# Optimization experiments

Hardware: AMD Instinct MI355X
Metric: run time of the kernel (lower is better)

## Reference

```python
import jax, jax.numpy as jnp
import numpy as np

B = 65536
D = 764  # n_dim


def setup_inputs() -> dict:
    key = jax.random.key(0)
    k1, k2, k3 = jax.random.split(key, 3)
    x = jax.random.normal(k1, (B, D), dtype=jnp.float32)
    # Packed weights: row i holds linear_layers[i].weight (length max(1,i), zero-padded).
    W = jax.random.normal(k2, (D, D), dtype=jnp.float32) * 0.02
    b = jax.random.normal(k3, (D,), dtype=jnp.float32) * 0.02
    return {"x": x, "W": W, "b": b}


def reference(x, W, b):
    # Original: output[i] = x[:, :i] @ W_i^T + b_i for i>=1; output[0] = b_0
    # (layer 0 is applied to an explicit zeros tensor, so its weight contributes nothing).
    # This is a single strictly-lower-triangular masked matmul.
    d = W.shape[0]
    mask = jnp.tril(jnp.ones((d, d), dtype=x.dtype), k=-1)  # row i uses cols < i
    return jnp.einsum('bd,nd->bn', x, W * mask) + b  # [B, n_dim]
```

## Files before the change

### kernel.cpp

```cpp
#include <hip/hip_runtime.h>

#define D_DIM 764
#define DP    768
#define BM    128
#define BN    128
#define BK    64

typedef __attribute__((ext_vector_type(8))) short bf16x8;
typedef __attribute__((ext_vector_type(8))) unsigned short u16x8;
typedef __attribute__((ext_vector_type(4))) float f32x4;

typedef __attribute__((address_space(3))) char lds_char;
typedef __attribute__((address_space(1))) const char g_char;

__device__ inline unsigned short f2bf(float f) {
    union { float f; unsigned u; } v; v.f = f;
    unsigned r = v.u + 0x7FFFu + ((v.u >> 16) & 1u);
    return (unsigned short)(r >> 16);
}

__global__ void prep_w(const float* __restrict__ W, unsigned short* __restrict__ Wb) {
    int idx = blockIdx.x * blockDim.x + threadIdx.x;
    int n = idx / DP, k = idx - n * DP;
    float v = 0.0f;
    if (n < D_DIM && k < n) v = W[n * D_DIM + k];
    Wb[idx] = f2bf(v);
}

__global__ __launch_bounds__(256, 4) void fvsbn_gemm(
    const float* __restrict__ X,
    const unsigned short* __restrict__ Wb,
    const float* __restrict__ bias,
    float* __restrict__ out)
{
    __shared__ __align__(16) unsigned short As[BM * BK];
    __shared__ __align__(16) unsigned short Bs[BN * BK];

    const int tid  = threadIdx.x;
    const int lane = tid & 63;
    const int wid  = tid >> 6;
    const int wm   = wid & 1;
    const int wn   = wid >> 1;
    const int quad = lane >> 4;
    const int l16  = lane & 15;

    const int bid = blockIdx.x;
    const int xcd = bid & 7;
    const int j   = bid >> 3;
    const int nt  = j % 6;
    const int jm  = j / 6;
    const int mt  = jm * 8 + xcd;
    const int m0  = mt * BM;
    const int n0  = nt * BN;

    const int num_k = (n0 + BN) / BK;

    f32x4 acc[4][4];
#pragma unroll
    for (int i = 0; i < 4; ++i)
#pragma unroll
        for (int jj = 0; jj < 4; ++jj) acc[i][jj] = (f32x4){0.f, 0.f, 0.f, 0.f};

    for (int kk = 0; kk < num_k; ++kk) {
        const int k0 = kk * BK;

#pragma unroll
        for (int jj = 0; jj < 4; ++jj) {
            const int cbase = (wid * 4 + jj) * 64;
            const int c     = cbase + lane;
            const int r     = c >> 3;
            const int cc    = c & 7;
            const int g     = cc ^ (r & 7);
            const unsigned short* gp = Wb + (size_t)(n0 + r) * DP + k0 + g * 8;
            __builtin_amdgcn_global_load_lds((g_char*)gp,
                                             (lds_char*)((char*)Bs + cbase * 16),
                                             16, 0, 0);
        }

#pragma unroll
        for (int i = 0; i < 4; ++i) {
            const int p  = tid + i * 256;
            const int r  = p >> 3;
            const int cc = p & 7;
            const int g  = cc ^ (r & 7);
            const int k  = k0 + g * 8;
            const float* xp = X + (size_t)(m0 + r) * D_DIM + k;
            float4 lo = *(const float4*)xp;
            float4 hi = (k + 8 <= D_DIM) ? *(const float4*)(xp + 4)
                                         : make_float4(0.f, 0.f, 0.f, 0.f);
            u16x8 pk;
            pk[0] = f2bf(lo.x); pk[1] = f2bf(lo.y); pk[2] = f2bf(lo.z); pk[3] = f2bf(lo.w);
            pk[4] = f2bf(hi.x); pk[5] = f2bf(hi.y); pk[6] = f2bf(hi.z); pk[7] = f2bf(hi.w);
            *(u16x8*)&As[r * BK + cc * 8] = pk;
        }

        __syncthreads();

#pragma unroll
        for (int s = 0; s < 2; ++s) {
            bf16x8 af[4], bfr[4];
#pragma unroll
            for (int mi = 0; mi < 4; ++mi) {
                const int r = wm * 64 + mi * 16 + l16;
                const int g = s * 4 + quad;
                af[mi] = *(const bf16x8*)&As[r * BK + (g ^ (r & 7)) * 8];
            }
#pragma unroll
            for (int ni = 0; ni < 4; ++ni) {
                const int r = wn * 64 + ni * 16 + l16;
                const int g = s * 4 + quad;
                bfr[ni] = *(const bf16x8*)&Bs[r * BK + (g ^ (r & 7)) * 8];
            }
#pragma unroll
            for (int mi = 0; mi < 4; ++mi)
#pragma unroll
                for (int ni = 0; ni < 4; ++ni)
                    acc[mi][ni] = __builtin_amdgcn_mfma_f32_16x16x32_bf16(
                        af[mi], bfr[ni], acc[mi][ni], 0, 0, 0);
        }

        __syncthreads();
    }

#pragma unroll
    for (int ni = 0; ni < 4; ++ni) {
        const int col = n0 + wn * 64 + ni * 16 + l16;
        if (col < D_DIM) {
            const float bv = bias[col];
#pragma unroll
            for (int mi = 0; mi < 4; ++mi) {
                const int row = m0 + wm * 64 + mi * 16 + quad * 4;
#pragma unroll
                for (int r = 0; r < 4; ++r)
                    out[(size_t)(row + r) * D_DIM + col] = acc[mi][ni][r] + bv;
            }
        }
    }
}

extern "C" void kernel_launch(void* const* d_in, const int* in_sizes, int n_in,
                              void* d_out, int out_size, void* d_ws, size_t ws_size,
                              hipStream_t stream) {
    const float* X    = (const float*)d_in[0];
    const float* W    = (const float*)d_in[1];
    const float* bias = (const float*)d_in[2];
    float* out        = (float*)d_out;
    unsigned short* Wb = (unsigned short*)d_ws;

    prep_w<<<(DP * DP) / 256, 256, 0, stream>>>(W, Wb);
    fvsbn_gemm<<<(65536 / BM) * (DP / BN), 256, 0, stream>>>(X, Wb, bias, out);
}
```

Before: 465.0 us.

## Double-buffer LDS tiles and use 8 waves per block for GEMM

Adds double-buffered LDS for the A and B tiles. The next k-tile's X loads and W global-to-LDS copies are issued before the MFMA compute on the current tile, and the bf16-converted A tile is written after compute, so only one barrier remains per iteration. The block grows from 256 to 512 threads, with each wave computing a 32x64 sub-tile instead of 64x64, which lowers per-wave accumulator registers. The cost is twice the LDS per block and smaller per-wave MFMA work, which can reduce reuse of the B fragments read from LDS.

After: 433.8 us. 6.7% less time.

```diff
diff --git a/kernel.cpp b/kernel.cpp
--- a/kernel.cpp
+++ b/kernel.cpp
@@ -27,20 +27,20 @@
     Wb[idx] = f2bf(v);
 }
 
-__global__ __launch_bounds__(256, 4) void fvsbn_gemm(
+__global__ __launch_bounds__(512, 4) void fvsbn_gemm(
     const float* __restrict__ X,
     const unsigned short* __restrict__ Wb,
     const float* __restrict__ bias,
     float* __restrict__ out)
 {
-    __shared__ __align__(16) unsigned short As[BM * BK];
-    __shared__ __align__(16) unsigned short Bs[BN * BK];
+    __shared__ __align__(16) unsigned short As[2][BM * BK];
+    __shared__ __align__(16) unsigned short Bs[2][BN * BK];
 
     const int tid  = threadIdx.x;
     const int lane = tid & 63;
     const int wid  = tid >> 6;
-    const int wm   = wid & 1;
-    const int wn   = wid >> 1;
+    const int wm   = wid & 3;
+    const int wn   = wid >> 2;
     const int quad = lane >> 4;
     const int l16  = lane & 15;
 
@@ -55,71 +55,107 @@
 
     const int num_k = (n0 + BN) / BK;
 
-    f32x4 acc[4][4];
+    const unsigned short* bsrc[2];
 #pragma unroll
-    for (int i = 0; i < 4; ++i)
+    for (int jj = 0; jj < 2; ++jj) {
+        const int c  = (wid * 2 + jj) * 64 + lane;
+        const int r  = c >> 3;
+        const int cc = c & 7;
+        const int g  = cc ^ (r & 7);
+        bsrc[jj] = Wb + (size_t)(n0 + r) * DP + g * 8;
+    }
+    const float* asrc[2];
+    int adst[2], hilim[2];
 #pragma unroll
-        for (int jj = 0; jj < 4; ++jj) acc[i][jj] = (f32x4){0.f, 0.f, 0.f, 0.f};
+    for (int i = 0; i < 2; ++i) {
+        const int p  = tid + i * 512;
+        const int r  = p >> 3;
+        const int cc = p & 7;
+        const int g  = cc ^ (r & 7);
+        asrc[i]  = X + (size_t)(m0 + r) * D_DIM + g * 8;
+        adst[i]  = r * BK + cc * 8;
+        hilim[i] = D_DIM - 8 - g * 8;
+    }
 
+    f32x4 acc[2][4];
+#pragma unroll
+    for (int mi = 0; mi < 2; ++mi)
+#pragma unroll
+        for (int ni = 0; ni < 4; ++ni) acc[mi][ni] = (f32x4){0.f, 0.f, 0.f, 0.f};
+
+    float4 xlo[2], xhi[2];
+
+#define LOAD_A(k0s)                                                         \
+    _Pragma("unroll")                                                       \
+    for (int i = 0; i < 2; ++i) {                                           \
+        const float* xp = asrc[i] + (k0s);                                  \
+        xlo[i] = *(const float4*)xp;                                        \
+        xhi[i] = ((k0s) <= hilim[i]) ? *(const float4*)(xp + 4)             \
+                                     : make_float4(0.f, 0.f, 0.f, 0.f);     \
+    }
+
+#define STAGE_B(buf, k0s)                                                   \
+    _Pragma("unroll")                                                       \
+    for (int jj = 0; jj < 2; ++jj) {                                        \
+        __builtin_amdgcn_global_load_lds(                                   \
+            (g_char*)(bsrc[jj] + (k0s)),                                    \
+            (lds_char*)((char*)&Bs[buf][0] + ((wid * 2 + jj) * 64) * 16),   \
+            16, 0, 0);                                                      \
+    }
+
+#define WRITE_A(buf)                                                        \
+    _Pragma("unroll")                                                       \
+    for (int i = 0; i < 2; ++i) {                                           \
+        u16x8 pk;                                                           \
+        pk[0] = f2bf(xlo[i].x); pk[1] = f2bf(xlo[i].y);                     \
+        pk[2] = f2bf(xlo[i].z); pk[3] = f2bf(xlo[i].w);                     \
+        pk[4] = f2bf(xhi[i].x); pk[5] = f2bf(xhi[i].y);                     \
+        pk[6] = f2bf(xhi[i].z); pk[7] = f2bf(xhi[i].w);                     \
+        *(u16x8*)&As[buf][adst[i]] = pk;                                    \
+    }
+
+#define COMPUTE(buf)                                                        \
+    _Pragma("unroll")                                                       \
+    for (int s = 0; s < 2; ++s) {                                           \
+        bf16x8 af[2], bfr[4];                                               \
+        _Pragma("unroll")                                                   \
+        for (int mi = 0; mi < 2; ++mi) {                                    \
+            const int r = wm * 32 + mi * 16 + l16;                          \
+            const int g = s * 4 + quad;                                     \
+            af[mi] = *(const bf16x8*)&As[buf][r * BK + (g ^ (r & 7)) * 8];  \
+        }                                                                   \
+        _Pragma("unroll")                                                   \
+        for (int ni = 0; ni < 4; ++ni) {                                    \
+            const int r = wn * 64 + ni * 16 + l16;                          \
+            const int g = s * 4 + quad;                                     \
+            bfr[ni] = *(const bf16x8*)&Bs[buf][r * BK + (g ^ (r & 7)) * 8]; \
+        }                                                                   \
+        _Pragma("unroll")                                                   \
+        for (int mi = 0; mi < 2; ++mi)                                      \
+            _Pragma("unroll")                                               \
+            for (int ni = 0; ni < 4; ++ni)                                  \
+                acc[mi][ni] = __builtin_amdgcn_mfma_f32_16x16x32_bf16(      \
+                    af[mi], bfr[ni], acc[mi][ni], 0, 0, 0);                 \
+    }
+
+    LOAD_A(0);
+    STAGE_B(0, 0);
+    WRITE_A(0);
+    __syncthreads();
+
+    int cur = 0;
     for (int kk = 0; kk < num_k; ++kk) {
-        const int k0 = kk * BK;
-
-#pragma unroll
-        for (int jj = 0; jj < 4; ++jj) {
-            const int cbase = (wid * 4 + jj) * 64;
-            const int c     = cbase + lane;
-            const int r     = c >> 3;
-            const int cc    = c & 7;
-            const int g     = cc ^ (r & 7);
-            const unsigned short* gp = Wb + (size_t)(n0 + r) * DP + k0 + g * 8;
-            __builtin_amdgcn_global_load_lds((g_char*)gp,
-                                             (lds_char*)((char*)Bs + cbase * 16),
-                                             16, 0, 0);
+        const int nxt  = cur ^ 1;
+        const bool more = (kk + 1 < num_k);
+        if (more) {
+            const int k0n = (kk + 1) * BK;
+            LOAD_A(k0n);
+            STAGE_B(nxt, k0n);
         }
-
-#pragma unroll
-        for (int i = 0; i < 4; ++i) {
-            const int p  = tid + i * 256;
-            const int r  = p >> 3;
-            const int cc = p & 7;
-            const int g  = cc ^ (r & 7);
-            const int k  = k0 + g * 8;
-            const float* xp = X + (size_t)(m0 + r) * D_DIM + k;
-            float4 lo = *(const float4*)xp;
-            float4 hi = (k + 8 <= D_DIM) ? *(const float4*)(xp + 4)
-                                         : make_float4(0.f, 0.f, 0.f, 0.f);
-            u16x8 pk;
-            pk[0] = f2bf(lo.x); pk[1] = f2bf(lo.y); pk[2] = f2bf(lo.z); pk[3] = f2bf(lo.w);
-            pk[4] = f2bf(hi.x); pk[5] = f2bf(hi.y); pk[6] = f2bf(hi.z); pk[7] = f2bf(hi.w);
-            *(u16x8*)&As[r * BK + cc * 8] = pk;
-        }
-
+        COMPUTE(cur);
+        if (more) WRITE_A(nxt);
         __syncthreads();
-
-#pragma unroll
-        for (int s = 0; s < 2; ++s) {
-            bf16x8 af[4], bfr[4];
-#pragma unroll
-            for (int mi = 0; mi < 4; ++mi) {
-                const int r = wm * 64 + mi * 16 + l16;
-                const int g = s * 4 + quad;
-                af[mi] = *(const bf16x8*)&As[r * BK + (g ^ (r & 7)) * 8];
-            }
-#pragma unroll
-            for (int ni = 0; ni < 4; ++ni) {
-                const int r = wn * 64 + ni * 16 + l16;
-                const int g = s * 4 + quad;
-                bfr[ni] = *(const bf16x8*)&Bs[r * BK + (g ^ (r & 7)) * 8];
-            }
-#pragma unroll
-            for (int mi = 0; mi < 4; ++mi)
-#pragma unroll
-                for (int ni = 0; ni < 4; ++ni)
-                    acc[mi][ni] = __builtin_amdgcn_mfma_f32_16x16x32_bf16(
-                        af[mi], bfr[ni], acc[mi][ni], 0, 0, 0);
-        }
-
-        __syncthreads();
+        cur = nxt;
     }
 
 #pragma unroll
@@ -128,14 +164,18 @@
         if (col < D_DIM) {
             const float bv = bias[col];
 #pragma unroll
-            for (int mi = 0; mi < 4; ++mi) {
-                const int row = m0 + wm * 64 + mi * 16 + quad * 4;
+            for (int mi = 0; mi < 2; ++mi) {
+                const int row = m0 + wm * 32 + mi * 16 + quad * 4;
 #pragma unroll
                 for (int r = 0; r < 4; ++r)
                     out[(size_t)(row + r) * D_DIM + col] = acc[mi][ni][r] + bv;
             }
         }
     }
+#undef LOAD_A
+#undef STAGE_B
+#undef WRITE_A
+#undef COMPUTE
 }
 
 extern "C" void kernel_launch(void* const* d_in, const int* in_sizes, int n_in,
@@ -148,5 +188,5 @@
     unsigned short* Wb = (unsigned short*)d_ws;
 
     prep_w<<<(DP * DP) / 256, 256, 0, stream>>>(W, Wb);
-    fvsbn_gemm<<<(65536 / BM) * (DP / BN), 256, 0, stream>>>(X, Wb, bias, out);
+    fvsbn_gemm<<<(65536 / BM) * (DP / BN), 512, 0, stream>>>(X, Wb, bias, out);
 }
```
